# Kernel optimization log

Hardware: AMD Instinct MI355X
Metric: run time of the kernel (lower is better)

Reference implementation:

```python
import jax, jax.numpy as jnp
import numpy as np

ROOT_2 = 1.41421
C = 256
DIV = 4
CP = C // DIV  # 64


def _spectral_normalize(w2d):
    # exact largest singular value (torch uses power iteration approx of this)
    s = jnp.linalg.norm(w2d, ord=2)
    return w2d / s


def setup_inputs() -> dict:
    key = jax.random.key(0)
    ks = jax.random.split(key, 10)
    B, H, W = 8, 64, 64
    x = jax.random.normal(ks[0], (B, C, H, W), dtype=jnp.float32)
    # 1x1 conv weights stored as [out, in]; spectral-normalized like torch's spectral_norm
    def conv_w(k, o, i):
        w = jax.random.normal(k, (o, i), dtype=jnp.float32) * (1.0 / np.sqrt(i))
        return _spectral_normalize(w)
    Wq = conv_w(ks[1], CP, C); bq = jnp.zeros((CP,), jnp.float32)
    Wk = conv_w(ks[2], CP, C); bk = jnp.zeros((CP,), jnp.float32)
    Wv = conv_w(ks[3], CP, C); bv = jnp.zeros((CP,), jnp.float32)
    Wo = conv_w(ks[4], C, CP); bo = jnp.zeros((C,), jnp.float32)
    gamma = jnp.zeros((1,), jnp.float32)
    return {"x": x, "Wq": Wq, "bq": bq, "Wk": Wk, "bk": bk,
            "Wv": Wv, "bv": bv, "Wo": Wo, "bo": bo, "gamma": gamma}


def reference(x, Wq, bq, Wk, bk, Wv, bv, Wo, bo, gamma):
    B, c, h, w = x.shape
    n = h * w
    const1 = jnp.float32(ROOT_2 / np.sqrt(C))       # Weight_Scaling(in_channels)
    const2 = jnp.float32(ROOT_2 / np.sqrt(CP))      # Weight_Scaling(in_channels//div_num)
    xs = (const1 * x).reshape(B, c, n)              # [B,C,N]
    q = jnp.einsum('oc,bcn->bon', Wq, xs) + bq[None, :, None]  # [B,C',N]
    k = jnp.einsum('oc,bcn->bon', Wk, xs) + bk[None, :, None]
    v = jnp.einsum('oc,bcn->bon', Wv, xs) + bv[None, :, None]
    # attn[b,i,j] = softmax_j(q[:,i]^T k[:,j])
    scores = jnp.einsum('bcn,bcm->bnm', q, k)       # [B,N,N]
    attn = jax.nn.softmax(scores, axis=-1)
    sa = jnp.einsum('bcm,bnm->bcn', v, attn)        # v @ attn^T
    sa = const2 * sa
    out = jnp.einsum('oc,bcn->bon', Wo, sa) + bo[None, :, None]  # [B,C,N]
    out = out.reshape(B, c, h, w)
    return gamma[0] * out + x
```

## Files before the change

kernel.cpp:

```cpp
#include <hip/hip_runtime.h>


#define Bsz 8
#define Cch 256
#define CPd 64
#define Nn  4096
#define TIL 64
#define NSPL 2
#define MHALF (Nn / NSPL)

typedef __attribute__((ext_vector_type(8))) short short8;
typedef __attribute__((ext_vector_type(4))) float f32x4;

static constexpr float C1 = (float)(1.41421 / 16.0);
static constexpr float C2 = (float)(1.41421 / 8.0);

__device__ inline unsigned pk_trunc(float lo, float hi) {
    return __builtin_amdgcn_perm(__float_as_uint(hi), __float_as_uint(lo), 0x07060302u);
}
__device__ inline float dpp_swap1(float v) {
    return __uint_as_float((unsigned)__builtin_amdgcn_mov_dpp(
        (int)__float_as_uint(v), 0xB1, 0xF, 0xF, true));
}

__global__ __launch_bounds__(256) void wconv_kernel(
    const float* __restrict__ Wq, const float* __restrict__ Wk,
    const float* __restrict__ Wv, const float* __restrict__ Wo,
    unsigned short* __restrict__ Wb)
{
    const int idx = (blockIdx.x * 256 + threadIdx.x) * 4;
    const float* src = (idx < 16384) ? Wq : (idx < 32768) ? Wk : (idx < 49152) ? Wv : Wo;
    const float4 v = *(const float4*)(src + (idx & 16383));
    *(uint2*)(Wb + idx) = make_uint2(pk_trunc(v.x, v.y), pk_trunc(v.z, v.w));
}

__global__ __launch_bounds__(256) void qkv_kernel(
    const float* __restrict__ x, const unsigned short* __restrict__ Wb,
    const float* __restrict__ bq, const float* __restrict__ bk, const float* __restrict__ bv,
    unsigned short* __restrict__ qT, unsigned short* __restrict__ kT,
    unsigned short* __restrict__ vB)
{
    __shared__ __align__(16) unsigned short Wlds[CPd * 264];
    __shared__ __align__(16) float T[TIL * 68];

    const int b   = blockIdx.y;
    const int n0  = blockIdx.x * TIL;
    const int t   = threadIdx.x;
    const int g   = t >> 6;
    const int l15 = t & 15;
    const int l4  = (t & 63) >> 4;

    const float* xb = x + (size_t)b * Cch * Nn + n0 + 16 * g + l15;
    short8 xf[8];
    #pragma unroll
    for (int ks = 0; ks < 8; ++ks) {
        float xr[8];
        #pragma unroll
        for (int j = 0; j < 8; ++j)
            xr[j] = C1 * xb[(size_t)(8 * l4 + 32 * ks + j) * Nn];
        union { unsigned u[4]; short8 s; } p;
        p.u[0] = pk_trunc(xr[0], xr[1]); p.u[1] = pk_trunc(xr[2], xr[3]);
        p.u[2] = pk_trunc(xr[4], xr[5]); p.u[3] = pk_trunc(xr[6], xr[7]);
        xf[ks] = p.s;
    }

    #pragma unroll
    for (int mat = 0; mat < 3; ++mat) {
        {
            const uint4* wg = (const uint4*)(Wb + mat * 16384);
            #pragma unroll
            for (int p = 0; p < 8; ++p) {
                const int idx = p * 256 + t;
                const int o = idx >> 5, cs = idx & 31;
                *(uint4*)&Wlds[o * 264 + cs * 8] = wg[idx];
            }
        }
        __syncthreads();

        const float* bias = (mat == 0) ? bq : (mat == 1) ? bk : bv;
        f32x4 acc[4];
        #pragma unroll
        for (int st = 0; st < 4; ++st) {
            const float bb = bias[16 * st + l15];
            acc[st] = (f32x4){bb, bb, bb, bb};
        }
        #pragma unroll
        for (int st = 0; st < 4; ++st) {
            #pragma unroll
            for (int ks = 0; ks < 8; ++ks) {
                const short8 wf = *(const short8*)&Wlds[(16 * st + l15) * 264 + 8 * l4 + 32 * ks];
                acc[st] = __builtin_amdgcn_mfma_f32_16x16x32_bf16(xf[ks], wf, acc[st], 0, 0, 0);
            }
        }
        __syncthreads();

        if (mat < 2) {
            #pragma unroll
            for (int st = 0; st < 4; ++st)
                #pragma unroll
                for (int r = 0; r < 4; ++r)
                    T[(16 * g + 4 * l4 + r) * 68 + 16 * st + l15] = acc[st][r];
        } else {
            #pragma unroll
            for (int st = 0; st < 4; ++st)
                #pragma unroll
                for (int r = 0; r < 4; ++r)
                    T[(16 * st + l15) * 68 + 16 * g + 4 * l4 + r] = acc[st][r];
        }
        __syncthreads();

        const int row = t >> 2;
        const int sg  = 16 * (t & 3);
        const float4 a0 = *(const float4*)&T[row * 68 + sg + 0];
        const float4 a1 = *(const float4*)&T[row * 68 + sg + 4];
        const float4 a2 = *(const float4*)&T[row * 68 + sg + 8];
        const float4 a3 = *(const float4*)&T[row * 68 + sg + 12];
        const uint4 lo = make_uint4(pk_trunc(a0.x, a0.y), pk_trunc(a0.z, a0.w),
                                    pk_trunc(a1.x, a1.y), pk_trunc(a1.z, a1.w));
        const uint4 hi = make_uint4(pk_trunc(a2.x, a2.y), pk_trunc(a2.z, a2.w),
                                    pk_trunc(a3.x, a3.y), pk_trunc(a3.z, a3.w));
        unsigned short* dst;
        if (mat < 2) {
            dst = (mat == 0 ? qT : kT) + ((size_t)(b * Nn + n0 + row)) * CPd + sg;
        } else {
            dst = vB + ((size_t)(b * CPd + row)) * Nn + n0 + sg;
        }
        *(uint4*)dst = lo;
        *(uint4*)(dst + 8) = hi;
    }
}

__global__ __launch_bounds__(256, 4) void flash_kernel(
    const unsigned short* __restrict__ qT, const unsigned short* __restrict__ kT,
    const unsigned short* __restrict__ vB, float* __restrict__ Op, float* __restrict__ Lg)
{
    __shared__ __align__(16) unsigned short Ks[TIL * 72];
    __shared__ __align__(16) unsigned short Vs[TIL * 72];
    __shared__ __align__(16) unsigned Pb[TIL * 36];
    __shared__ float Lsh[TIL];

    const int b   = blockIdx.y;
    const int n0  = blockIdx.x * TIL;
    const int s   = blockIdx.z;
    const int t   = threadIdx.x;
    const int l   = t & 63;
    const int g   = t >> 6;
    const int l15 = l & 15;
    const int l4  = l >> 4;
    const int par = l & 1;
    const unsigned sel = par ? 0x03020706u : 0x07060302u;
    const int l15h = l15 >> 1;

    if (t < TIL) Lsh[t] = 0.f;

    const unsigned short* qp = qT + (size_t)(b * Nn + n0 + 16 * g + l15) * CPd + 8 * l4;
    const short8 qf0 = *(const short8*)qp;
    const short8 qf1 = *(const short8*)(qp + 32);

    f32x4 acco[4];
    #pragma unroll
    for (int ct = 0; ct < 4; ++ct) acco[ct] = (f32x4){0.f, 0.f, 0.f, 0.f};
    float Lp[4] = {0.f, 0.f, 0.f, 0.f};

    const uint4* kg = (const uint4*)(kT + (size_t)b * Nn * CPd);
    const unsigned short* vb = vB + (size_t)b * CPd * Nn;
    const int mbase = s * MHALF;

    for (int mi = 0; mi < MHALF; mi += TIL) {
        const int m0 = mbase + mi;
        __syncthreads();
        {
            const int r = t >> 3, cc = t & 7;
            uint4 k0 = kg[(m0 + r) * 8 + cc];
            uint4 k1 = kg[(m0 + r + 32) * 8 + cc];
            *(uint4*)&Ks[r * 72 + 8 * cc]        = k0;
            *(uint4*)&Ks[(r + 32) * 72 + 8 * cc] = k1;
            uint4 w0 = *(const uint4*)(vb + (size_t)r * Nn + m0 + 8 * cc);
            uint4 w1 = *(const uint4*)(vb + (size_t)(r + 32) * Nn + m0 + 8 * cc);
            *(uint4*)&Vs[r * 72 + 8 * cc]        = w0;
            *(uint4*)&Vs[(r + 32) * 72 + 8 * cc] = w1;
        }
        __syncthreads();

        f32x4 accs[4];
        #pragma unroll
        for (int st = 0; st < 4; ++st) {
            accs[st] = (f32x4){0.f, 0.f, 0.f, 0.f};
            const short8 kf0 = *(const short8*)&Ks[(16 * st + l15) * 72 + 8 * l4];
            const short8 kf1 = *(const short8*)&Ks[(16 * st + l15) * 72 + 8 * l4 + 32];
            accs[st] = __builtin_amdgcn_mfma_f32_16x16x32_bf16(qf0, kf0, accs[st], 0, 0, 0);
            accs[st] = __builtin_amdgcn_mfma_f32_16x16x32_bf16(qf1, kf1, accs[st], 0, 0, 0);
        }

        #pragma unroll
        for (int st = 0; st < 4; ++st) {
            unsigned u[4];
            #pragma unroll
            for (int r = 0; r < 4; ++r) {
                float p = __expf(accs[st][r]);
                Lp[r] += p;
                float nb = dpp_swap1(p);
                u[r] = __builtin_amdgcn_perm(__float_as_uint(nb), __float_as_uint(p), sel);
            }
            const int rb = 16 * g + 4 * l4 + 2 * par;
            Pb[(rb + 0) * 36 + 8 * st + l15h] = u[2 * par];
            Pb[(rb + 1) * 36 + 8 * st + l15h] = u[2 * par + 1];
        }
        __syncthreads();

        #pragma unroll
        for (int ks = 0; ks < 2; ++ks) {
            const short8 pf = *(const short8*)&Pb[(16 * g + l15) * 36 + 4 * l4 + 16 * ks];
            #pragma unroll
            for (int ct = 0; ct < 4; ++ct) {
                const short8 vf = *(const short8*)&Vs[(16 * ct + l15) * 72 + 8 * l4 + 32 * ks];
                acco[ct] = __builtin_amdgcn_mfma_f32_16x16x32_bf16(pf, vf, acco[ct], 0, 0, 0);
            }
        }
    }

    #pragma unroll
    for (int r = 0; r < 4; ++r) atomicAdd(&Lsh[16 * g + 4 * l4 + r], Lp[r]);
    __syncthreads();

    float* ob = Op + ((size_t)(s * Bsz + b) * Nn + n0) * CPd;
    #pragma unroll
    for (int r = 0; r < 4; ++r) {
        const int nl = 16 * g + 4 * l4 + r;
        #pragma unroll
        for (int ct = 0; ct < 4; ++ct)
            ob[(size_t)nl * CPd + 16 * ct + l15] = acco[ct][r];
    }
    if (t < TIL) Lg[(size_t)(s * Bsz + b) * Nn + n0 + t] = Lsh[t];
}

__global__ __launch_bounds__(512) void out_kernel(
    const float* __restrict__ Op, const float* __restrict__ Lg,
    const unsigned short* __restrict__ Wob,
    const float* __restrict__ bo, const float* __restrict__ gamma,
    const float* __restrict__ x, float* __restrict__ y)
{
    __shared__ __align__(16) unsigned short Wos[Cch * 72];
    __shared__ __align__(16) unsigned short Sas[TIL * 72];
    __shared__ float bos[Cch];

    const int b   = blockIdx.y;
    const int n0  = blockIdx.x * TIL;
    const int t   = threadIdx.x;
    const int l   = t & 63;
    const int w   = t >> 6;
    const int l15 = l & 15;
    const int l4  = l >> 4;

    if (t < Cch) bos[t] = bo[t];
    {
        const uint4* wg = (const uint4*)Wob;
        #pragma unroll
        for (int p = 0; p < 4; ++p) {
            const int idx = p * 512 + t;
            const int row = idx >> 3, seg = idx & 7;
            *(uint4*)&Wos[row * 72 + seg * 8] = wg[idx];
        }
    }
    if (t < 256) {
        const int n = t >> 2, seg = t & 3;
        const float* o0 = Op + ((size_t)(b * Nn + n0 + n)) * CPd + seg * 16;
        const float* o1 = o0 + (size_t)Bsz * Nn * CPd;
        const float l0 = Lg[(size_t)b * Nn + n0 + n];
        const float l1 = Lg[(size_t)(Bsz + b) * Nn + n0 + n];
        const float sc = C2 / (l0 + l1);
        unsigned pk[8];
        #pragma unroll
        for (int i = 0; i < 4; ++i) {
            const float4 a = ((const float4*)o0)[i];
            const float4 c = ((const float4*)o1)[i];
            pk[2 * i]     = pk_trunc((a.x + c.x) * sc, (a.y + c.y) * sc);
            pk[2 * i + 1] = pk_trunc((a.z + c.z) * sc, (a.w + c.w) * sc);
        }
        *(uint4*)&Sas[n * 72 + seg * 16]     = make_uint4(pk[0], pk[1], pk[2], pk[3]);
        *(uint4*)&Sas[n * 72 + seg * 16 + 8] = make_uint4(pk[4], pk[5], pk[6], pk[7]);
    }
    __syncthreads();

    short8 bfr[4][2];
    #pragma unroll
    for (int ns = 0; ns < 4; ++ns) {
        bfr[ns][0] = *(const short8*)&Sas[(16 * ns + l15) * 72 + 8 * l4];
        bfr[ns][1] = *(const short8*)&Sas[(16 * ns + l15) * 72 + 8 * l4 + 32];
    }
    const float gam = gamma[0];
    const float* xb = x + (size_t)b * Cch * Nn;
    float*       yb = y + (size_t)b * Cch * Nn;

    #pragma unroll
    for (int os2 = 0; os2 < 2; ++os2) {
        const int obase = 16 * (w + 8 * os2);
        const short8 af0 = *(const short8*)&Wos[(obase + l15) * 72 + 8 * l4];
        const short8 af1 = *(const short8*)&Wos[(obase + l15) * 72 + 8 * l4 + 32];
        #pragma unroll
        for (int ns = 0; ns < 4; ++ns) {
            f32x4 acc = (f32x4){0.f, 0.f, 0.f, 0.f};
            acc = __builtin_amdgcn_mfma_f32_16x16x32_bf16(af0, bfr[ns][0], acc, 0, 0, 0);
            acc = __builtin_amdgcn_mfma_f32_16x16x32_bf16(af1, bfr[ns][1], acc, 0, 0, 0);
            #pragma unroll
            for (int r = 0; r < 4; ++r) {
                const int o = obase + 4 * l4 + r;
                const size_t idx = (size_t)o * Nn + n0 + 16 * ns + l15;
                yb[idx] = fmaf(gam, acc[r] + bos[o], xb[idx]);
            }
        }
    }
}

extern "C" void kernel_launch(void* const* d_in, const int* in_sizes, int n_in,
                              void* d_out, int out_size, void* d_ws, size_t ws_size,
                              hipStream_t stream)
{
    (void)in_sizes; (void)n_in; (void)out_size; (void)ws_size;
    const float* x     = (const float*)d_in[0];
    const float* Wq    = (const float*)d_in[1];
    const float* bq    = (const float*)d_in[2];
    const float* Wk    = (const float*)d_in[3];
    const float* bk    = (const float*)d_in[4];
    const float* Wv    = (const float*)d_in[5];
    const float* bv    = (const float*)d_in[6];
    const float* Wo    = (const float*)d_in[7];
    const float* bo    = (const float*)d_in[8];
    const float* gamma = (const float*)d_in[9];
    float* y = (float*)d_out;

    const size_t per = (size_t)Bsz * Nn * CPd;
    unsigned short* qT = (unsigned short*)d_ws;
    unsigned short* kT = qT + per;
    unsigned short* vB = kT + per;
    float* Op = (float*)(vB + per);
    float* Lg = Op + NSPL * per;
    unsigned short* Wb = (unsigned short*)(Lg + NSPL * Bsz * Nn);

    dim3 grid(Nn / TIL, Bsz);
    dim3 gridF(Nn / TIL, Bsz, NSPL);
    wconv_kernel<<<64, 256, 0, stream>>>(Wq, Wk, Wv, Wo, Wb);
    qkv_kernel<<<grid, 256, 0, stream>>>(x, Wb, bq, bk, bv, qT, kT, vB);
    flash_kernel<<<gridF, 256, 0, stream>>>(qT, kT, vB, Op, Lg);
    out_kernel<<<grid, 512, 0, stream>>>(Op, Lg, Wb + 3 * 16384, bo, gamma, x, y);
}
```

Baseline: 187.6 us.

## Use 32x32x16 MFMA tiles in flash kernel and stage x transpose via LDS

The flash kernel moves from 16x16x32 MFMAs, where each wave owns 16 query rows, to 32x32x16 MFMAs laid out as a 2x2 wave grid over query and key/value halves. Each wave keeps two interleaved accumulators to break MFMA dependency chains, and the P buffer pitch changes to match the new write pattern. The qkv kernel now loads x with coalesced float4 reads, packs it to bf16, and transposes it through LDS instead of doing strided scalar global loads. This adds extra barriers and raises register use in exchange for better MFMA efficiency and load coalescing.

```diff
diff --git a/kernel.cpp b/kernel.cpp
--- a/kernel.cpp
+++ b/kernel.cpp
@@ -9,8 +9,9 @@
 #define NSPL 2
 #define MHALF (Nn / NSPL)
 
-typedef __attribute__((ext_vector_type(8))) short short8;
-typedef __attribute__((ext_vector_type(4))) float f32x4;
+typedef __attribute__((ext_vector_type(8)))  short short8;
+typedef __attribute__((ext_vector_type(4)))  float f32x4;
+typedef __attribute__((ext_vector_type(16))) float f32x16;
 
 static constexpr float C1 = (float)(1.41421 / 16.0);
 static constexpr float C2 = (float)(1.41421 / 8.0);
@@ -40,8 +41,8 @@
     unsigned short* __restrict__ qT, unsigned short* __restrict__ kT,
     unsigned short* __restrict__ vB)
 {
+    __shared__ __align__(16) unsigned XsT[TIL * 132];
     __shared__ __align__(16) unsigned short Wlds[CPd * 264];
-    __shared__ __align__(16) float T[TIL * 68];
 
     const int b   = blockIdx.y;
     const int n0  = blockIdx.x * TIL;
@@ -50,19 +51,32 @@
     const int l15 = t & 15;
     const int l4  = (t & 63) >> 4;
 
-    const float* xb = x + (size_t)b * Cch * Nn + n0 + 16 * g + l15;
+    {
+        const float* xb = x + (size_t)b * Cch * Nn + n0;
+        const int tc = t & 15;
+        const int tn = t >> 4;
+        #pragma unroll
+        for (int cc = 0; cc < 8; ++cc) {
+            const int cp = tc + 16 * cc;
+            const float4 f0 = *(const float4*)(xb + (size_t)(2 * cp + 0) * Nn + 4 * tn);
+            const float4 f1 = *(const float4*)(xb + (size_t)(2 * cp + 1) * Nn + 4 * tn);
+            XsT[(4 * tn + 0) * 132 + cp] = pk_trunc(C1 * f0.x, C1 * f1.x);
+            XsT[(4 * tn + 1) * 132 + cp] = pk_trunc(C1 * f0.y, C1 * f1.y);
+            XsT[(4 * tn + 2) * 132 + cp] = pk_trunc(C1 * f0.z, C1 * f1.z);
+            XsT[(4 * tn + 3) * 132 + cp] = pk_trunc(C1 * f0.w, C1 * f1.w);
+        }
+    }
+    __syncthreads();
+
     short8 xf[8];
-    #pragma unroll
-    for (int ks = 0; ks < 8; ++ks) {
-        float xr[8];
-        #pragma unroll
-        for (int j = 0; j < 8; ++j)
-            xr[j] = C1 * xb[(size_t)(8 * l4 + 32 * ks + j) * Nn];
-        union { unsigned u[4]; short8 s; } p;
-        p.u[0] = pk_trunc(xr[0], xr[1]); p.u[1] = pk_trunc(xr[2], xr[3]);
-        p.u[2] = pk_trunc(xr[4], xr[5]); p.u[3] = pk_trunc(xr[6], xr[7]);
-        xf[ks] = p.s;
-    }
+    {
+        const unsigned short* xrow = (const unsigned short*)&XsT[(16 * g + l15) * 132];
+        #pragma unroll
+        for (int ks = 0; ks < 8; ++ks) xf[ks] = *(const short8*)(xrow + 8 * l4 + 32 * ks);
+    }
+    __syncthreads();
+
+    float* T = (float*)XsT;
 
     #pragma unroll
     for (int mat = 0; mat < 3; ++mat) {
@@ -127,6 +141,7 @@
         }
         *(uint4*)dst = lo;
         *(uint4*)(dst + 8) = hi;
+        __syncthreads();
     }
 }
 
@@ -136,7 +151,7 @@
 {
     __shared__ __align__(16) unsigned short Ks[TIL * 72];
     __shared__ __align__(16) unsigned short Vs[TIL * 72];
-    __shared__ __align__(16) unsigned Pb[TIL * 36];
+    __shared__ __align__(16) unsigned Pb[TIL * 40];
     __shared__ float Lsh[TIL];
 
     const int b   = blockIdx.y;
@@ -144,26 +159,31 @@
     const int s   = blockIdx.z;
     const int t   = threadIdx.x;
     const int l   = t & 63;
-    const int g   = t >> 6;
-    const int l15 = l & 15;
-    const int l4  = l >> 4;
-    const int par = l & 1;
-    const unsigned sel = par ? 0x03020706u : 0x07060302u;
-    const int l15h = l15 >> 1;
+    const int w   = t >> 6;
+    const int nh  = w & 1;
+    const int mq  = w >> 1;
+    const int l31 = l & 31;
+    const int l1  = l >> 5;
 
     if (t < TIL) Lsh[t] = 0.f;
 
-    const unsigned short* qp = qT + (size_t)(b * Nn + n0 + 16 * g + l15) * CPd + 8 * l4;
-    const short8 qf0 = *(const short8*)qp;
-    const short8 qf1 = *(const short8*)(qp + 32);
-
-    f32x4 acco[4];
-    #pragma unroll
-    for (int ct = 0; ct < 4; ++ct) acco[ct] = (f32x4){0.f, 0.f, 0.f, 0.f};
-    float Lp[4] = {0.f, 0.f, 0.f, 0.f};
+    short8 qf[4];
+    {
+        const unsigned short* qp = qT + (size_t)(b * Nn + n0 + 32 * nh + l31) * CPd + 8 * l1;
+        #pragma unroll
+        for (int kc = 0; kc < 4; ++kc) qf[kc] = *(const short8*)(qp + 16 * kc);
+    }
+
+    f32x16 acco_a, acco_b;
+    float Lp[16];
+    #pragma unroll
+    for (int r = 0; r < 16; ++r) { acco_a[r] = 0.f; acco_b[r] = 0.f; Lp[r] = 0.f; }
 
     const uint4* kg = (const uint4*)(kT + (size_t)b * Nn * CPd);
     const unsigned short* vb = vB + (size_t)b * CPd * Nn;
+    const unsigned sel = (l & 1) ? 0x03020706u : 0x07060302u;
+    const int par  = l & 1;
+    const int colp = 16 * mq + (l31 >> 1);
     const int mbase = s * MHALF;
 
     for (int mi = 0; mi < MHALF; mi += TIL) {
@@ -182,54 +202,64 @@
         }
         __syncthreads();
 
-        f32x4 accs[4];
-        #pragma unroll
-        for (int st = 0; st < 4; ++st) {
-            accs[st] = (f32x4){0.f, 0.f, 0.f, 0.f};
-            const short8 kf0 = *(const short8*)&Ks[(16 * st + l15) * 72 + 8 * l4];
-            const short8 kf1 = *(const short8*)&Ks[(16 * st + l15) * 72 + 8 * l4 + 32];
-            accs[st] = __builtin_amdgcn_mfma_f32_16x16x32_bf16(qf0, kf0, accs[st], 0, 0, 0);
-            accs[st] = __builtin_amdgcn_mfma_f32_16x16x32_bf16(qf1, kf1, accs[st], 0, 0, 0);
-        }
-
-        #pragma unroll
-        for (int st = 0; st < 4; ++st) {
-            unsigned u[4];
-            #pragma unroll
-            for (int r = 0; r < 4; ++r) {
-                float p = __expf(accs[st][r]);
-                Lp[r] += p;
-                float nb = dpp_swap1(p);
-                u[r] = __builtin_amdgcn_perm(__float_as_uint(nb), __float_as_uint(p), sel);
+        f32x16 sa, sb;
+        #pragma unroll
+        for (int r = 0; r < 16; ++r) { sa[r] = 0.f; sb[r] = 0.f; }
+        {
+            const short8 kf0 = *(const short8*)&Ks[(32 * mq + l31) * 72 + 8 * l1];
+            const short8 kf1 = *(const short8*)&Ks[(32 * mq + l31) * 72 + 16 + 8 * l1];
+            const short8 kf2 = *(const short8*)&Ks[(32 * mq + l31) * 72 + 32 + 8 * l1];
+            const short8 kf3 = *(const short8*)&Ks[(32 * mq + l31) * 72 + 48 + 8 * l1];
+            sa = __builtin_amdgcn_mfma_f32_32x32x16_bf16(qf[0], kf0, sa, 0, 0, 0);
+            sb = __builtin_amdgcn_mfma_f32_32x32x16_bf16(qf[1], kf1, sb, 0, 0, 0);
+            sa = __builtin_amdgcn_mfma_f32_32x32x16_bf16(qf[2], kf2, sa, 0, 0, 0);
+            sb = __builtin_amdgcn_mfma_f32_32x32x16_bf16(qf[3], kf3, sb, 0, 0, 0);
+        }
+
+        unsigned u[16];
+        #pragma unroll
+        for (int r = 0; r < 16; ++r) {
+            float p = __expf(sa[r] + sb[r]);
+            Lp[r] += p;
+            float nb = dpp_swap1(p);
+            u[r] = __builtin_amdgcn_perm(__float_as_uint(nb), __float_as_uint(p), sel);
+        }
+        {
+            const int rb = 32 * nh + 4 * l1 + 2 * par;
+            #pragma unroll
+            for (int q = 0; q < 4; ++q) {
+                Pb[(rb + 8 * q) * 40 + colp]     = u[4 * q + 2 * par];
+                Pb[(rb + 8 * q + 1) * 40 + colp] = u[4 * q + 2 * par + 1];
             }
-            const int rb = 16 * g + 4 * l4 + 2 * par;
-            Pb[(rb + 0) * 36 + 8 * st + l15h] = u[2 * par];
-            Pb[(rb + 1) * 36 + 8 * st + l15h] = u[2 * par + 1];
-        }
-        __syncthreads();
-
-        #pragma unroll
-        for (int ks = 0; ks < 2; ++ks) {
-            const short8 pf = *(const short8*)&Pb[(16 * g + l15) * 36 + 4 * l4 + 16 * ks];
-            #pragma unroll
-            for (int ct = 0; ct < 4; ++ct) {
-                const short8 vf = *(const short8*)&Vs[(16 * ct + l15) * 72 + 8 * l4 + 32 * ks];
-                acco[ct] = __builtin_amdgcn_mfma_f32_16x16x32_bf16(pf, vf, acco[ct], 0, 0, 0);
-            }
-        }
-    }
-
-    #pragma unroll
-    for (int r = 0; r < 4; ++r) atomicAdd(&Lsh[16 * g + 4 * l4 + r], Lp[r]);
+        }
+        __syncthreads();
+
+        {
+            const short8 pf0 = *(const short8*)&Pb[(32 * nh + l31) * 40 + 4 * l1];
+            const short8 vf0 = *(const short8*)&Vs[(32 * mq + l31) * 72 + 8 * l1];
+            acco_a = __builtin_amdgcn_mfma_f32_32x32x16_bf16(pf0, vf0, acco_a, 0, 0, 0);
+            const short8 pf1 = *(const short8*)&Pb[(32 * nh + l31) * 40 + 8 + 4 * l1];
+            const short8 vf1 = *(const short8*)&Vs[(32 * mq + l31) * 72 + 16 + 8 * l1];
+            acco_b = __builtin_amdgcn_mfma_f32_32x32x16_bf16(pf1, vf1, acco_b, 0, 0, 0);
+            const short8 pf2 = *(const short8*)&Pb[(32 * nh + l31) * 40 + 16 + 4 * l1];
+            const short8 vf2 = *(const short8*)&Vs[(32 * mq + l31) * 72 + 32 + 8 * l1];
+            acco_a = __builtin_amdgcn_mfma_f32_32x32x16_bf16(pf2, vf2, acco_a, 0, 0, 0);
+            const short8 pf3 = *(const short8*)&Pb[(32 * nh + l31) * 40 + 24 + 4 * l1];
+            const short8 vf3 = *(const short8*)&Vs[(32 * mq + l31) * 72 + 48 + 8 * l1];
+            acco_b = __builtin_amdgcn_mfma_f32_32x32x16_bf16(pf3, vf3, acco_b, 0, 0, 0);
+        }
+    }
+
+    #pragma unroll
+    for (int r = 0; r < 16; ++r)
+        atomicAdd(&Lsh[32 * nh + (r & 3) + 8 * (r >> 2) + 4 * l1], Lp[r]);
     __syncthreads();
 
     float* ob = Op + ((size_t)(s * Bsz + b) * Nn + n0) * CPd;
     #pragma unroll
-    for (int r = 0; r < 4; ++r) {
-        const int nl = 16 * g + 4 * l4 + r;
-        #pragma unroll
-        for (int ct = 0; ct < 4; ++ct)
-            ob[(size_t)nl * CPd + 16 * ct + l15] = acco[ct][r];
+    for (int r = 0; r < 16; ++r) {
+        const int nl = 32 * nh + (r & 3) + 8 * (r >> 2) + 4 * l1;
+        ob[(size_t)nl * CPd + 32 * mq + l31] = acco_a[r] + acco_b[r];
     }
     if (t < TIL) Lg[(size_t)(s * Bsz + b) * Nn + n0 + t] = Lsh[t];
 }
```

Result: slower. 241.6 us (+28.8%).
